# Kernel tuning notes

Hardware: AMD Instinct MI355X
Metric: run time of the kernel (lower is better)

## Reference

```python
import jax, jax.numpy as jnp
import numpy as np

H, I_, N, K, R, NL = 768, 1536, 16, 4, 48, 8
B, L, DIN = 4, 1024, 13
DA, RP = 128, 4
EPS = 1e-5

def _rmsnorm(x, w):
    v = jnp.mean(jnp.square(x), axis=-1, keepdims=True)
    return x * jax.lax.rsqrt(v + EPS) * w

def _causal_dwconv(hs, w, b):
    # hs: [B, I, L]; w: [I, K] depthwise kernel; causal (left) padding = K-1
    out = jax.lax.conv_general_dilated(
        hs, w[:, None, :], window_strides=(1,), padding=[(K - 1, 0)],
        dimension_numbers=('NCH', 'OIH', 'NCH'), feature_group_count=hs.shape[1])
    return out + b[None, :, None]

def _selective_scan(u, dt, Bm, Cm, A, D):
    # u, dt: [B, L, I]; Bm, Cm: [B, L, N]; A: [I, N]; D: [I]
    def step(h, inp):
        dt_t, B_t, C_t, u_t = inp          # [B,I], [B,N], [B,N], [B,I]
        dA = jnp.exp(dt_t[:, :, None] * A)  # [B,I,N]
        h = dA * h + (dt_t * u_t)[:, :, None] * B_t[:, None, :]
        y = jnp.einsum('bin,bn->bi', h, C_t)
        return h, y
    h0 = jnp.zeros((u.shape[0], A.shape[0], A.shape[1]), u.dtype)
    xs = (jnp.swapaxes(dt, 0, 1), jnp.swapaxes(Bm, 0, 1),
          jnp.swapaxes(Cm, 0, 1), jnp.swapaxes(u, 0, 1))
    _, ys = jax.lax.scan(step, h0, xs)
    return jnp.swapaxes(ys, 0, 1) + u * D

def _mamba_block(x, norm_w, in_w, conv_w, conv_b, xproj_w, dt_w, dt_b, A_log, D, out_w):
    res = x
    h = _rmsnorm(x, norm_w)
    proj = h @ in_w.T                      # [B,L,2I]
    hs, gate = jnp.split(proj, 2, axis=-1)
    hs = jnp.swapaxes(hs, 1, 2)            # [B,I,L]
    hs = jax.nn.silu(_causal_dwconv(hs, conv_w, conv_b))
    u = jnp.swapaxes(hs, 1, 2)             # [B,L,I]
    ssm = u @ xproj_w.T                    # [B,L,R+2N]
    ts, Bm, Cm = ssm[..., :R], ssm[..., R:R + N], ssm[..., R + N:]
    dt = jax.nn.softplus(ts @ dt_w.T + dt_b)
    y = _selective_scan(u, dt, Bm, Cm, -jnp.exp(A_log), D)
    y = y * jax.nn.silu(gate)
    return res + y @ out_w.T

def _forward(x, mlp_in_w1, mlp_in_b1, mlp_in_w2, mlp_in_b2, mlp_in_w3, mlp_in_b3,
             layers_norm_w, layers_in_proj_w, layers_conv_w, layers_conv_b,
             layers_x_proj_w, layers_dt_w, layers_dt_b, layers_A_log, layers_D,
             layers_out_proj_w, norm_f_w, attn_ws1, attn_ws2,
             mlp_out_w1, mlp_out_b1, mlp_out_w2, mlp_out_b2, mlp_out_w3, mlp_out_b3):
    h = jax.nn.relu(x @ mlp_in_w1.T + mlp_in_b1)
    h = jax.nn.relu(h @ mlp_in_w2.T + mlp_in_b2)
    h = h @ mlp_in_w3.T + mlp_in_b3        # [B,L,H]
    for l in range(NL):
        h = _mamba_block(h, layers_norm_w[l], layers_in_proj_w[l], layers_conv_w[l],
                         layers_conv_b[l], layers_x_proj_w[l], layers_dt_w[l],
                         layers_dt_b[l], layers_A_log[l], layers_D[l],
                         layers_out_proj_w[l])
    h = _rmsnorm(h, norm_f_w)              # final norm_f
    # attention pooling: softmax over the sequence dim (dim=1)
    attn = jax.nn.softmax(jnp.tanh(h @ attn_ws1.T) @ attn_ws2.T, axis=1)  # [B,L,r]
    m = jnp.einsum('blr,blh->brh', attn, h)  # bmm(attn^T, h) -> [B,r,H]
    flat = m.reshape(m.shape[0], -1)         # [B, r*H]
    o = jax.nn.relu(flat @ mlp_out_w1.T + mlp_out_b1)
    o = jax.nn.relu(o @ mlp_out_w2.T + mlp_out_b2)
    return o @ mlp_out_w3.T + mlp_out_b3     # [B,1]

def setup_inputs():
    key = jax.random.key(0)
    ks = iter(jax.random.split(key, 40))
    def nrm(shape, s=0.02):
        return jax.random.normal(next(ks), shape, dtype=jnp.float32) * s
    A_log = jnp.log(jnp.tile(jnp.arange(1, N + 1, dtype=jnp.float32)[None, None, :], (NL, I_, 1)))
    return {
        'x': jax.random.normal(next(ks), (B, L, DIN), dtype=jnp.float32),
        'mlp_in_w1': nrm((256, DIN)), 'mlp_in_b1': jnp.zeros((256,), jnp.float32),
        'mlp_in_w2': nrm((256, 256)), 'mlp_in_b2': jnp.zeros((256,), jnp.float32),
        'mlp_in_w3': nrm((H, 256)), 'mlp_in_b3': jnp.zeros((H,), jnp.float32),
        'layers_norm_w': jnp.ones((NL, H), jnp.float32),
        'layers_in_proj_w': nrm((NL, 2 * I_, H)),
        'layers_conv_w': nrm((NL, I_, K), 0.1),
        'layers_conv_b': jnp.zeros((NL, I_), jnp.float32),
        'layers_x_proj_w': nrm((NL, R + 2 * N, I_)),
        'layers_dt_w': nrm((NL, I_, R)),
        'layers_dt_b': jnp.full((NL, I_), -4.6, jnp.float32),
        'layers_A_log': A_log,
        'layers_D': jnp.ones((NL, I_), jnp.float32),
        'layers_out_proj_w': nrm((NL, H, I_)),
        'norm_f_w': jnp.ones((H,), jnp.float32),
        'attn_ws1': nrm((DA, H)), 'attn_ws2': nrm((RP, DA)),
        'mlp_out_w1': nrm((256, H * RP)), 'mlp_out_b1': jnp.zeros((256,), jnp.float32),
        'mlp_out_w2': nrm((256, 256)), 'mlp_out_b2': jnp.zeros((256,), jnp.float32),
        'mlp_out_w3': nrm((1, 256)), 'mlp_out_b3': jnp.zeros((1,), jnp.float32),
    }

def reference(x, mlp_in_w1, mlp_in_b1, mlp_in_w2, mlp_in_b2, mlp_in_w3, mlp_in_b3,
              layers_norm_w, layers_in_proj_w, layers_conv_w, layers_conv_b,
              layers_x_proj_w, layers_dt_w, layers_dt_b, layers_A_log, layers_D,
              layers_out_proj_w, norm_f_w, attn_ws1, attn_ws2,
              mlp_out_w1, mlp_out_b1, mlp_out_w2, mlp_out_b2, mlp_out_w3, mlp_out_b3):
    return _forward(x, mlp_in_w1, mlp_in_b1, mlp_in_w2, mlp_in_b2, mlp_in_w3, mlp_in_b3,
                    layers_norm_w, layers_in_proj_w, layers_conv_w, layers_conv_b,
                    layers_x_proj_w, layers_dt_w, layers_dt_b, layers_A_log, layers_D,
                    layers_out_proj_w, norm_f_w, attn_ws1, attn_ws2,
                    mlp_out_w1, mlp_out_b1, mlp_out_w2, mlp_out_b2, mlp_out_w3, mlp_out_b3)
```

## Files before the change

### kernel.cpp

```cpp
#include <hip/hip_runtime.h>
#include <cstddef>
#include <cstdint>

#define HD    768
#define ID    1536
#define ND    16
#define KD    4
#define RD    48
#define NLAY  8
#define BB    4
#define LL    1024
#define BL    4096
#define DIN   13
#define DA_   128
#define RP_   4

#define NC    32
#define CS    32

typedef _Float16 f16;
typedef f16 f16x8 __attribute__((ext_vector_type(8)));
typedef float f32x4 __attribute__((ext_vector_type(4)));

__device__ __forceinline__ float softplus_f(float x) {
    return (x > 20.f) ? x : log1pf(expf(x));
}

__device__ __forceinline__ float fast_exp2(float x) {
#if __has_builtin(__builtin_amdgcn_exp2f)
    return __builtin_amdgcn_exp2f(x);
#else
    return exp2f(x);
#endif
}

__global__ __launch_bounds__(256) void cast_f16_k(
    const float* __restrict__ in, f16* __restrict__ out, int n)
{
    int i = (blockIdx.x * 256 + threadIdx.x) * 4;
    if (i + 3 < n) {
        float4 v = *(const float4*)(in + i);
        out[i]     = (f16)v.x;
        out[i + 1] = (f16)v.y;
        out[i + 2] = (f16)v.z;
        out[i + 3] = (f16)v.w;
    } else {
        for (int j = i; j < n; ++j) out[j] = (f16)in[j];
    }
}

__global__ __launch_bounds__(256) void cast_dtw_k(
    const float* __restrict__ in, f16* __restrict__ out)
{
    int idx = blockIdx.x * 256 + threadIdx.x;
    if (idx >= NLAY * ID * 64) return;
    int k = idx & 63, r = idx >> 6;
    out[idx] = (k < RD) ? (f16)in[r * RD + k] : (f16)0.f;
}

__global__ __launch_bounds__(256) void zero_k(float* __restrict__ p, int n)
{
    int i = blockIdx.x * 256 + threadIdx.x;
    if (i < n) p[i] = 0.f;
}

__device__ __forceinline__ void epilogue_store(
    float v, int row, int col, int N,
    const float* __restrict__ res, int ldres,
    float* __restrict__ C, int ldc,
    f16* __restrict__ Cb, int ldcb, int ncb, int act,
    const float* __restrict__ bias)
{
    if (col >= N) return;
    if (bias) v += bias[col];
    if (act == 1) v = fmaxf(v, 0.f);
    else if (act == 2) v = tanhf(v);
    else if (act == 3) v = softplus_f(v);
    if (res) v += res[(size_t)row * ldres + col];
    if (C) C[(size_t)row * ldc + col] = v;
    if (Cb && col < ncb) Cb[(size_t)row * ldcb + col] = (f16)v;
}

__device__ __forceinline__ void async_copy16(const f16* g, f16* l) {
    __builtin_amdgcn_global_load_lds(
        (const __attribute__((address_space(1))) void*)g,
        (__attribute__((address_space(3))) void*)l, 16, 0, 0);
}

__global__ __launch_bounds__(256) void hgemm_k(
    const f16* __restrict__ A, int lda,
    const f16* __restrict__ W, int ldw,
    const float* __restrict__ bias,
    const float* __restrict__ res, int ldres,
    float* __restrict__ C, int ldc,
    f16* __restrict__ Cb, int ldcb, int ncb,
    int M, int N, int K, int act)
{
    __shared__ f16 As[128 * 64];
    __shared__ f16 Bs[128 * 64];
    int tid = threadIdx.x;
    int wave = tid >> 6, lane = tid & 63;
    int m0 = blockIdx.y * 128, n0 = blockIdx.x * 128;

    int wm = wave & 1, wn = wave >> 1;
    int lm = lane & 15;
    int kq = (lane >> 4) * 8;

    int srow = tid >> 2;
    int skc  = (tid & 3) * 8;

    f32x4 acc[4][4] = {};

    for (int k0 = 0; k0 < K; k0 += 64) {
#pragma unroll
        for (int it = 0; it < 4; ++it) {
            int rowo = (it & 1) * 64 + srow;
            int kk   = (it >> 1) * 32 + skc;
            int base = (it >> 1) * 4096 + (it & 1) * 2048 + wave * 512;
            async_copy16(A + (size_t)(m0 + rowo) * lda + k0 + kk, As + base);
            async_copy16(W + (size_t)(n0 + rowo) * ldw + k0 + kk, Bs + base);
        }
        __syncthreads();

        f16x8 af[4][2], bf[4][2];
#pragma unroll
        for (int ks = 0; ks < 2; ++ks) {
#pragma unroll
            for (int mt = 0; mt < 4; ++mt)
                af[mt][ks] = *(const f16x8*)(As + ks * 4096 +
                                 (wm * 64 + mt * 16 + lm) * 32 + kq);
#pragma unroll
            for (int nt = 0; nt < 4; ++nt)
                bf[nt][ks] = *(const f16x8*)(Bs + ks * 4096 +
                                 (wn * 64 + nt * 16 + lm) * 32 + kq);
        }
#pragma unroll
        for (int ks = 0; ks < 2; ++ks)
#pragma unroll
            for (int mt = 0; mt < 4; ++mt)
#pragma unroll
                for (int nt = 0; nt < 4; ++nt)
                    acc[mt][nt] = __builtin_amdgcn_mfma_f32_16x16x32_f16(
                        af[mt][ks], bf[nt][ks], acc[mt][nt], 0, 0, 0);
        __syncthreads();
    }

    int rq = (lane >> 4) * 4;
#pragma unroll
    for (int mt = 0; mt < 4; ++mt)
#pragma unroll
        for (int nt = 0; nt < 4; ++nt) {
            int col = n0 + wn * 64 + nt * 16 + lm;
#pragma unroll
            for (int r = 0; r < 4; ++r) {
                int row = m0 + wm * 64 + mt * 16 + rq + r;
                epilogue_store(acc[mt][nt][r], row, col, N, res, ldres,
                               C, ldc, Cb, ldcb, ncb, act, bias);
            }
        }
}

__global__ __launch_bounds__(256) void hgemm64_k(
    const f16* __restrict__ A, int lda,
    const f16* __restrict__ W, int ldw,
    const float* __restrict__ bias,
    const float* __restrict__ res, int ldres,
    float* __restrict__ C, int ldc,
    f16* __restrict__ Cb, int ldcb, int ncb,
    int M, int N, int K, int act)
{
    __shared__ f16 As[64 * 64];
    __shared__ f16 Bs[64 * 64];
    int tid = threadIdx.x;
    int wave = tid >> 6, lane = tid & 63;
    int m0 = blockIdx.y * 64, n0 = blockIdx.x * 64;

    int wm = wave & 1, wn = wave >> 1;
    int lm = lane & 15;
    int kq = (lane >> 4) * 8;

    int srow = tid >> 2;
    int skc  = (tid & 3) * 8;

    f32x4 acc[2][2] = {};

    for (int k0 = 0; k0 < K; k0 += 64) {
#pragma unroll
        for (int it = 0; it < 2; ++it) {
            int kk   = it * 32 + skc;
            int base = it * 2048 + wave * 512;
            async_copy16(A + (size_t)(m0 + srow) * lda + k0 + kk, As + base);
            async_copy16(W + (size_t)(n0 + srow) * ldw + k0 + kk, Bs + base);
        }
        __syncthreads();

        f16x8 af[2][2], bf[2][2];
#pragma unroll
        for (int ks = 0; ks < 2; ++ks) {
#pragma unroll
            for (int mt = 0; mt < 2; ++mt)
                af[mt][ks] = *(const f16x8*)(As + ks * 2048 +
                                 (wm * 32 + mt * 16 + lm) * 32 + kq);
#pragma unroll
            for (int nt = 0; nt < 2; ++nt)
                bf[nt][ks] = *(const f16x8*)(Bs + ks * 2048 +
                                 (wn * 32 + nt * 16 + lm) * 32 + kq);
        }
#pragma unroll
        for (int ks = 0; ks < 2; ++ks)
#pragma unroll
            for (int mt = 0; mt < 2; ++mt)
#pragma unroll
                for (int nt = 0; nt < 2; ++nt)
                    acc[mt][nt] = __builtin_amdgcn_mfma_f32_16x16x32_f16(
                        af[mt][ks], bf[nt][ks], acc[mt][nt], 0, 0, 0);
        __syncthreads();
    }

    int rq = (lane >> 4) * 4;
#pragma unroll
    for (int mt = 0; mt < 2; ++mt)
#pragma unroll
        for (int nt = 0; nt < 2; ++nt) {
            int col = n0 + wn * 32 + nt * 16 + lm;
#pragma unroll
            for (int r = 0; r < 4; ++r) {
                int row = m0 + wm * 32 + mt * 16 + rq + r;
                epilogue_store(acc[mt][nt][r], row, col, N, res, ldres,
                               C, ldc, Cb, ldcb, ncb, act, bias);
            }
        }
}

__global__ __launch_bounds__(256) void hgemm64s_k(
    const f16* __restrict__ A, int lda,
    const f16* __restrict__ W, int ldw,
    float* __restrict__ Cp, int ldc, size_t PS,
    int N, int kPer)
{
    __shared__ f16 As[64 * 64];
    __shared__ f16 Bs[64 * 64];
    int tid = threadIdx.x;
    int wave = tid >> 6, lane = tid & 63;
    int m0 = blockIdx.y * 64, n0 = blockIdx.x * 64;
    int z = blockIdx.z;
    int kbeg = z * kPer, kend = kbeg + kPer;

    int wm = wave & 1, wn = wave >> 1;
    int lm = lane & 15;
    int kq = (lane >> 4) * 8;
    int srow = tid >> 2;
    int skc  = (tid & 3) * 8;

    f32x4 acc[2][2] = {};

    for (int k0 = kbeg; k0 < kend; k0 += 64) {
#pragma unroll
        for (int it = 0; it < 2; ++it) {
            int kk   = it * 32 + skc;
            int base = it * 2048 + wave * 512;
            async_copy16(A + (size_t)(m0 + srow) * lda + k0 + kk, As + base);
            async_copy16(W + (size_t)(n0 + srow) * ldw + k0 + kk, Bs + base);
        }
        __syncthreads();

        f16x8 af[2][2], bf[2][2];
#pragma unroll
        for (int ks = 0; ks < 2; ++ks) {
#pragma unroll
            for (int mt = 0; mt < 2; ++mt)
                af[mt][ks] = *(const f16x8*)(As + ks * 2048 +
                                 (wm * 32 + mt * 16 + lm) * 32 + kq);
#pragma unroll
            for (int nt = 0; nt < 2; ++nt)
                bf[nt][ks] = *(const f16x8*)(Bs + ks * 2048 +
                                 (wn * 32 + nt * 16 + lm) * 32 + kq);
        }
#pragma unroll
        for (int ks = 0; ks < 2; ++ks)
#pragma unroll
            for (int mt = 0; mt < 2; ++mt)
#pragma unroll
                for (int nt = 0; nt < 2; ++nt)
                    acc[mt][nt] = __builtin_amdgcn_mfma_f32_16x16x32_f16(
                        af[mt][ks], bf[nt][ks], acc[mt][nt], 0, 0, 0);
        __syncthreads();
    }

    float* C = Cp + (size_t)z * PS;
    int rq = (lane >> 4) * 4;
#pragma unroll
    for (int mt = 0; mt < 2; ++mt)
#pragma unroll
        for (int nt = 0; nt < 2; ++nt) {
            int col = n0 + wn * 32 + nt * 16 + lm;
            if (col >= N) continue;
#pragma unroll
            for (int r = 0; r < 4; ++r) {
                int row = m0 + wm * 32 + mt * 16 + rq + r;
                C[(size_t)row * ldc + col] = acc[mt][nt][r];
            }
        }
}

__global__ __launch_bounds__(256) void xcomb_k(
    const float* __restrict__ part, float* __restrict__ ssm,
    f16* __restrict__ ssmb)
{
    int idx = blockIdx.x * 256 + threadIdx.x;
    if (idx >= BL * 96) return;
    int row = idx / 96, c = idx % 96;
    const size_t PS = (size_t)BL * 80;
    if (c < 80) {
        size_t o = (size_t)row * 80 + c;
        float s = part[o] + part[PS + o] + part[2 * PS + o] + part[3 * PS + o];
        ssm[o] = s;
        if (c < RD) ssmb[(size_t)row * 64 + c] = (f16)s;
    } else {
        ssmb[(size_t)row * 64 + (c - 80 + RD)] = (f16)0.f;
    }
}

#define BM 64
#define BN 64
#define BKK 16
__global__ __launch_bounds__(256) void gemm_k(
    const float* __restrict__ A, int lda,
    const float* __restrict__ W,
    const float* __restrict__ bias,
    float* __restrict__ C, int ldc,
    f16* __restrict__ Cb, int ldcb,
    int M, int N, int K, int act)
{
    __shared__ float As[BKK][BM + 4];
    __shared__ float Ws[BKK][BN + 4];
    int tid = threadIdx.x;
    int tx = tid & 15, ty = tid >> 4;
    int m0 = blockIdx.y * BM, n0 = blockIdx.x * BN;
    float acc[4][4] = {};
    int arow = tid >> 2;
    int acol = (tid & 3) * 4;

    for (int k0 = 0; k0 < K; k0 += BKK) {
        int gm = m0 + arow;
        int gn = n0 + arow;
#pragma unroll
        for (int j = 0; j < 4; ++j) {
            int gk = k0 + acol + j;
            float av = 0.f, wv = 0.f;
            if (gm < M && gk < K) av = A[(size_t)gm * lda + gk];
            if (gn < N && gk < K) wv = W[(size_t)gn * K + gk];
            As[acol + j][arow] = av;
            Ws[acol + j][arow] = wv;
        }
        __syncthreads();
#pragma unroll
        for (int k = 0; k < BKK; ++k) {
            float a[4], b[4];
#pragma unroll
            for (int i = 0; i < 4; ++i) a[i] = As[k][ty * 4 + i];
#pragma unroll
            for (int j = 0; j < 4; ++j) b[j] = Ws[k][tx * 4 + j];
#pragma unroll
            for (int i = 0; i < 4; ++i)
#pragma unroll
                for (int j = 0; j < 4; ++j)
                    acc[i][j] += a[i] * b[j];
        }
        __syncthreads();
    }

#pragma unroll
    for (int i = 0; i < 4; ++i) {
        int row = m0 + ty * 4 + i;
        if (row >= M) continue;
#pragma unroll
        for (int j = 0; j < 4; ++j) {
            int col = n0 + tx * 4 + j;
            if (col >= N) continue;
            float v = acc[i][j];
            if (bias) v += bias[col];
            if (act == 1) v = fmaxf(v, 0.f);
            if (C) C[(size_t)row * ldc + col] = v;
            if (Cb) Cb[(size_t)row * ldcb + col] = (f16)v;
        }
    }
}

__global__ __launch_bounds__(256) void rmsnorm_k(
    const float* __restrict__ x, const float* __restrict__ w,
    f16* __restrict__ out)
{
    int row = blockIdx.x;
    const float* xr = x + (size_t)row * HD;
    int tid = threadIdx.x;
    float v0 = xr[tid], v1 = xr[tid + 256], v2 = xr[tid + 512];
    __shared__ float red[256];
    red[tid] = v0 * v0 + v1 * v1 + v2 * v2;
    __syncthreads();
    for (int o = 128; o; o >>= 1) {
        if (tid < o) red[tid] += red[tid + o];
        __syncthreads();
    }
    float scale = rsqrtf(red[0] / (float)HD + 1e-5f);
    f16* outr = out + (size_t)row * HD;
    outr[tid]       = (f16)(v0 * scale * w[tid]);
    outr[tid + 256] = (f16)(v1 * scale * w[tid + 256]);
    outr[tid + 512] = (f16)(v2 * scale * w[tid + 512]);
}

__global__ __launch_bounds__(256) void conv_silu_k(
    const f16* __restrict__ projb, const float* __restrict__ cw,
    const float* __restrict__ cb, f16* __restrict__ ub)
{
    int idx = blockIdx.x * 256 + threadIdx.x;
    if (idx >= BL * (ID / 8)) return;
    int i8  = (idx % (ID / 8)) * 8;
    int row = idx / (ID / 8);
    int t = row & (LL - 1);

    float4 wv[8];
#pragma unroll
    for (int j = 0; j < 8; ++j)
        wv[j] = *(const float4*)(cw + (i8 + j) * KD);

    float s[8];
    float4 cb0 = *(const float4*)(cb + i8);
    float4 cb1 = *(const float4*)(cb + i8 + 4);
    s[0] = cb0.x; s[1] = cb0.y; s[2] = cb0.z; s[3] = cb0.w;
    s[4] = cb1.x; s[5] = cb1.y; s[6] = cb1.z; s[7] = cb1.w;

#pragma unroll
    for (int k = 0; k < KD; ++k) {
        int tt = t - (KD - 1) + k;
        if (tt < 0) continue;
        f16x8 p = *(const f16x8*)(projb + (size_t)(row - (KD - 1) + k) * (2 * ID) + i8);
#pragma unroll
        for (int j = 0; j < 8; ++j) {
            float wk = (k == 0) ? wv[j].x : (k == 1) ? wv[j].y
                     : (k == 2) ? wv[j].z : wv[j].w;
            s[j] += (float)p[j] * wk;
        }
    }
    f16x8 o;
#pragma unroll
    for (int j = 0; j < 8; ++j) {
        float v = s[j] / (1.f + expf(-s[j]));
        o[j] = (f16)v;
    }
    *(f16x8*)(ub + (size_t)row * ID + i8) = o;
}

__global__ __launch_bounds__(256) void scan1_k(
    const f16*   __restrict__ dtf,
    const float* __restrict__ ssm,
    const f16*   __restrict__ ub,
    const float* __restrict__ A_log,
    float* __restrict__ Pw, float* __restrict__ Hw)
{
    int b = blockIdx.z, c = blockIdx.y;
    int i = blockIdx.x * 256 + threadIdx.x;
    __shared__ float sB[CS * 16];
    for (int idx = threadIdx.x; idx < CS * 16; idx += 256) {
        int t = idx >> 4, n = idx & 15;
        sB[idx] = ssm[((size_t)(b * LL + c * CS + t)) * 80 + 48 + n];
    }
    __syncthreads();

    float Ain[16];
#pragma unroll
    for (int n = 0; n < 16; ++n)
        Ain[n] = -expf(A_log[i * ND + n]) * 1.44269504f;

    float h[16];
    float sdt = 0.f;
#pragma unroll
    for (int n = 0; n < 16; ++n) h[n] = 0.f;

    for (int t = 0; t < CS; ++t) {
        size_t row = (size_t)(b * LL + c * CS + t);
        float dtv = (float)dtf[row * ID + i];
        float x = dtv * (float)ub[row * ID + i];
        sdt += dtv;
        const float4* Bv = (const float4*)(sB + t * 16);
        float4 B0 = Bv[0], B1 = Bv[1], B2 = Bv[2], B3 = Bv[3];
        float Bf[16] = {B0.x, B0.y, B0.z, B0.w, B1.x, B1.y, B1.z, B1.w,
                        B2.x, B2.y, B2.z, B2.w, B3.x, B3.y, B3.z, B3.w};
#pragma unroll
        for (int n = 0; n < 16; ++n) {
            float dA = fast_exp2(dtv * Ain[n]);
            h[n] = dA * h[n] + x * Bf[n];
        }
    }
    size_t off = (((size_t)(b * NC + c) * ID + i) << 4);
    float4* pw = (float4*)(Pw + off);
    float4* hw = (float4*)(Hw + off);
#pragma unroll
    for (int q = 0; q < 4; ++q) {
        pw[q] = make_float4(fast_exp2(sdt * Ain[q*4]),
                            fast_exp2(sdt * Ain[q*4+1]),
                            fast_exp2(sdt * Ain[q*4+2]),
                            fast_exp2(sdt * Ain[q*4+3]));
        hw[q] = make_float4(h[q*4], h[q*4+1], h[q*4+2], h[q*4+3]);
    }
}

__global__ __launch_bounds__(256) void scan_comb_k(
    const float* __restrict__ Pw, float* __restrict__ Hw)
{
    int idx = blockIdx.x * 256 + threadIdx.x;
    int rem = idx & (ID * 16 - 1);
    int b = idx / (ID * 16);
    size_t base = (size_t)b * NC * ID * 16 + rem;
    float e = 0.f;
    for (int c = 0; c < NC; ++c) {
        size_t off = base + (size_t)c * ID * 16;
        float Hc = Hw[off];
        float Pc = Pw[off];
        Hw[off] = e;
        e = Hc + Pc * e;
    }
}

__global__ __launch_bounds__(256) void scan2_k(
    const f16*   __restrict__ dtf,
    const float* __restrict__ ssm,
    const f16*   __restrict__ ub,
    const f16*   __restrict__ projb,
    const float* __restrict__ A_log,
    const float* __restrict__ D,
    const float* __restrict__ Hw,
    f16* __restrict__ y)
{
    int b = blockIdx.z, c = blockIdx.y;
    int i = blockIdx.x * 256 + threadIdx.x;
    __shared__ float sB[CS * 16];
    __shared__ float sC[CS * 16];
    for (int idx = threadIdx.x; idx < CS * 16; idx += 256) {
        int t = idx >> 4, n = idx & 15;
        size_t row = (size_t)(b * LL + c * CS + t);
        sB[idx] = ssm[row * 80 + 48 + n];
        sC[idx] = ssm[row * 80 + 64 + n];
    }
    __syncthreads();

    float Ain[16];
#pragma unroll
    for (int n = 0; n < 16; ++n)
        Ain[n] = -expf(A_log[i * ND + n]) * 1.44269504f;
    float Dv = D[i];

    float h[16];
    size_t off = (((size_t)(b * NC + c) * ID + i) << 4);
    const float4* hw = (const float4*)(Hw + off);
#pragma unroll
    for (int q = 0; q < 4; ++q) {
        float4 v = hw[q];
        h[q*4] = v.x; h[q*4+1] = v.y; h[q*4+2] = v.z; h[q*4+3] = v.w;
    }

    for (int t = 0; t < CS; ++t) {
        size_t row = (size_t)(b * LL + c * CS + t);
        float dtv = (float)dtf[row * ID + i];
        float uv  = (float)ub[row * ID + i];
        float g   = (float)projb[row * (2 * ID) + ID + i];
        float x = dtv * uv;
        const float4* Bv = (const float4*)(sB + t * 16);
        const float4* Cv = (const float4*)(sC + t * 16);
        float4 B0 = Bv[0], B1 = Bv[1], B2 = Bv[2], B3 = Bv[3];
        float4 C0 = Cv[0], C1 = Cv[1], C2 = Cv[2], C3 = Cv[3];
        float Bf[16] = {B0.x, B0.y, B0.z, B0.w, B1.x, B1.y, B1.z, B1.w,
                        B2.x, B2.y, B2.z, B2.w, B3.x, B3.y, B3.z, B3.w};
        float Cf[16] = {C0.x, C0.y, C0.z, C0.w, C1.x, C1.y, C1.z, C1.w,
                        C2.x, C2.y, C2.z, C2.w, C3.x, C3.y, C3.z, C3.w};
        float yv = 0.f;
#pragma unroll
        for (int n = 0; n < 16; ++n) {
            float dA = fast_exp2(dtv * Ain[n]);
            h[n] = dA * h[n] + x * Bf[n];
            yv += h[n] * Cf[n];
        }
        yv = (yv + uv * Dv) * (g / (1.f + expf(-g)));
        y[row * ID + i] = (f16)yv;
    }
}

__global__ __launch_bounds__(256) void softmax_k(
    const float* __restrict__ s, float* __restrict__ attn)
{
    int b = blockIdx.x >> 2, r = blockIdx.x & 3;
    int tid = threadIdx.x;
    __shared__ float red[256];
    float mx = -1e30f;
    for (int j = 0; j < 4; ++j) {
        int t = tid + j * 256;
        mx = fmaxf(mx, s[((size_t)(b * LL + t)) * RP_ + r]);
    }
    red[tid] = mx;
    __syncthreads();
    for (int o = 128; o; o >>= 1) {
        if (tid < o) red[tid] = fmaxf(red[tid], red[tid + o]);
        __syncthreads();
    }
    mx = red[0];
    __syncthreads();
    float ev[4], sum = 0.f;
    for (int j = 0; j < 4; ++j) {
        int t = tid + j * 256;
        ev[j] = expf(s[((size_t)(b * LL + t)) * RP_ + r] - mx);
        sum += ev[j];
    }
    red[tid] = sum;
    __syncthreads();
    for (int o = 128; o; o >>= 1) {
        if (tid < o) red[tid] += red[tid + o];
        __syncthreads();
    }
    float inv = 1.f / red[0];
    for (int j = 0; j < 4; ++j) {
        int t = tid + j * 256;
        attn[((size_t)(b * LL + t)) * RP_ + r] = ev[j] * inv;
    }
}

__global__ __launch_bounds__(256) void pool_k(
    const float* __restrict__ attn, const f16* __restrict__ hn,
    float* __restrict__ m)
{
    int br = blockIdx.x;
    int b = br >> 2, r = br & 3;
    int t0 = blockIdx.y * 64;
    int tid = threadIdx.x;
    float acc0 = 0.f, acc1 = 0.f, acc2 = 0.f;
    for (int t = t0; t < t0 + 64; ++t) {
        float w = attn[((size_t)(b * LL + t)) * RP_ + r];
        const f16* hr = hn + ((size_t)(b * LL + t)) * HD;
        acc0 += w * (float)hr[tid];
        acc1 += w * (float)hr[tid + 256];
        acc2 += w * (float)hr[tid + 512];
    }
    float* outp = m + ((size_t)(b * RP_ + r)) * HD;
    atomicAdd(outp + tid, acc0);
    atomicAdd(outp + tid + 256, acc1);
    atomicAdd(outp + tid + 512, acc2);
}

__global__ __launch_bounds__(64) void gemv_k(
    const float* __restrict__ A, int lda,
    const float* __restrict__ W, const float* __restrict__ bias,
    float* __restrict__ C, int ldc, int K, int relu)
{
    int n = blockIdx.x, b = blockIdx.y;
    int lane = threadIdx.x;
    const float* a = A + (size_t)b * lda;
    const float* w = W + (size_t)n * K;
    float s = 0.f;
    for (int k = lane; k < K; k += 64) s += a[k] * w[k];
    for (int off = 32; off; off >>= 1) s += __shfl_down(s, off);
    if (lane == 0) {
        float v = s + (bias ? bias[n] : 0.f);
        if (relu) v = fmaxf(v, 0.f);
        C[(size_t)b * ldc + n] = v;
    }
}

extern "C" void kernel_launch(void* const* d_in, const int* in_sizes, int n_in,
                              void* d_out, int out_size, void* d_ws, size_t ws_size,
                              hipStream_t stream) {
    const float* x          = (const float*)d_in[0];
    const float* mlp_in_w1  = (const float*)d_in[1];
    const float* mlp_in_b1  = (const float*)d_in[2];
    const float* mlp_in_w2  = (const float*)d_in[3];
    const float* mlp_in_b2  = (const float*)d_in[4];
    const float* mlp_in_w3  = (const float*)d_in[5];
    const float* mlp_in_b3  = (const float*)d_in[6];
    const float* norm_w     = (const float*)d_in[7];
    const float* in_proj_w  = (const float*)d_in[8];
    const float* conv_w     = (const float*)d_in[9];
    const float* conv_b     = (const float*)d_in[10];
    const float* x_proj_w   = (const float*)d_in[11];
    const float* dt_w       = (const float*)d_in[12];
    const float* dt_b       = (const float*)d_in[13];
    const float* A_log      = (const float*)d_in[14];
    const float* Dp         = (const float*)d_in[15];
    const float* out_proj_w = (const float*)d_in[16];
    const float* norm_f_w   = (const float*)d_in[17];
    const float* attn_ws1   = (const float*)d_in[18];
    const float* attn_ws2   = (const float*)d_in[19];
    const float* mlp_out_w1 = (const float*)d_in[20];
    const float* mlp_out_b1 = (const float*)d_in[21];
    const float* mlp_out_w2 = (const float*)d_in[22];
    const float* mlp_out_b2 = (const float*)d_in[23];
    const float* mlp_out_w3 = (const float*)d_in[24];
    const float* mlp_out_b3 = (const float*)d_in[25];
    float* out = (float*)d_out;

    float* ws    = (float*)d_ws;
    float* h     = ws;
    float* ssm   = h    + (size_t)BL * HD;
    float* xpart = ssm  + (size_t)BL * 80;
    float* h1a   = xpart+ (size_t)4 * BL * 80;
    float* sbuf  = h1a  + (size_t)BL * DA_;
    float* attn  = sbuf + (size_t)BL * 4;
    float* mbuf  = attn + (size_t)BL * 4;
    float* o1    = mbuf + (size_t)BB * RP_ * HD;
    float* o2    = o1   + (size_t)BB * 256;
    float* Pw    = o2   + (size_t)BB * 256;
    float* Hw    = Pw   + (size_t)BB * NC * ID * 16;
    f16* fb    = (f16*)(Hw + (size_t)BB * NC * ID * 16);
    f16* h1b   = fb;
    f16* h2b   = h1b  + (size_t)BL * 256;
    f16* hnb   = h2b  + (size_t)BL * 256;
    f16* projb = hnb  + (size_t)BL * HD;
    f16* ub    = projb+ (size_t)BL * 2 * ID;
    f16* ssmb  = ub   + (size_t)BL * ID;
    f16* dtf   = ssmb + (size_t)BL * 64;
    f16* ybb   = dtf  + (size_t)BL * ID;
    f16* opwf  = ybb  + (size_t)BL * ID;
    f16* xpwf  = opwf + (size_t)NLAY * HD * ID;
    f16* dwwf  = xpwf + (size_t)NLAY * 80 * ID;
    f16* w2f   = dwwf + (size_t)NLAY * ID * 64;
    f16* w3f   = w2f  + 256 * 256;
    f16* a1f   = w3f  + HD * 256;
    f16* ipwf  = a1f  + DA_ * HD;

    size_t used_bytes = (size_t)((char*)(ipwf) - (char*)d_ws);
    size_t slot_bytes = (size_t)2 * ID * HD * sizeof(f16);
    int full = (ws_size >= used_bytes + (size_t)NLAY * slot_bytes) ? 1 : 0;

    dim3 blk(256);
    auto cgrid = [](int n) { return dim3((n / 4 + 255) / 256); };

    cast_f16_k<<<cgrid(256 * 256), blk, 0, stream>>>(mlp_in_w2, w2f, 256 * 256);
    cast_f16_k<<<cgrid(HD * 256), blk, 0, stream>>>(mlp_in_w3, w3f, HD * 256);
    cast_f16_k<<<cgrid(DA_ * HD), blk, 0, stream>>>(attn_ws1, a1f, DA_ * HD);
    cast_f16_k<<<cgrid(NLAY * HD * ID), blk, 0, stream>>>(out_proj_w, opwf, NLAY * HD * ID);
    cast_f16_k<<<cgrid(NLAY * 80 * ID), blk, 0, stream>>>(x_proj_w, xpwf, NLAY * 80 * ID);
    cast_dtw_k<<<(NLAY * ID * 64 + 255) / 256, blk, 0, stream>>>(dt_w, dwwf);
    if (full)
        cast_f16_k<<<cgrid(NLAY * 2 * ID * HD), blk, 0, stream>>>(
            in_proj_w, ipwf, NLAY * 2 * ID * HD);

    gemm_k<<<dim3(4, 64), blk, 0, stream>>>(
        x, DIN, mlp_in_w1, mlp_in_b1, nullptr, 0, h1b, 256, BL, 256, DIN, 1);
    hgemm64_k<<<dim3(4, 64), blk, 0, stream>>>(
        h1b, 256, w2f, 256, mlp_in_b2, nullptr, 0, nullptr, 0, h2b, 256, 256,
        BL, 256, 256, 1);
    hgemm64_k<<<dim3(12, 64), blk, 0, stream>>>(
        h2b, 256, w3f, 256, mlp_in_b3, nullptr, 0, h, HD, nullptr, 0, 0,
        BL, HD, 256, 0);

    for (int l = 0; l < NLAY; ++l) {
        const float* nw  = norm_w + (size_t)l * HD;
        const float* cw  = conv_w + (size_t)l * ID * KD;
        const float* cb  = conv_b + (size_t)l * ID;
        const float* db  = dt_b   + (size_t)l * ID;
        const float* al  = A_log  + (size_t)l * ID * ND;
        const float* dv  = Dp     + (size_t)l * ID;

        const f16* ipw;
        if (full) {
            ipw = ipwf + (size_t)l * 2 * ID * HD;
        } else {
            cast_f16_k<<<cgrid(2 * ID * HD), blk, 0, stream>>>(
                in_proj_w + (size_t)l * 2 * ID * HD, ipwf, 2 * ID * HD);
            ipw = ipwf;
        }
        rmsnorm_k<<<BL, blk, 0, stream>>>(h, nw, hnb);
        hgemm_k<<<dim3(24, 32), blk, 0, stream>>>(
            hnb, HD, ipw, HD, nullptr, nullptr, 0, nullptr, 0,
            projb, 2 * ID, 2 * ID, BL, 2 * ID, HD, 0);
        conv_silu_k<<<(BL * (ID / 8) + 255) / 256, blk, 0, stream>>>(
            projb, cw, cb, ub);

        hgemm64s_k<<<dim3(2, 64, 4), blk, 0, stream>>>(
            ub, ID, xpwf + (size_t)l * 80 * ID, ID,
            xpart, 80, (size_t)BL * 80, 80, ID / 4);
        xcomb_k<<<(BL * 96 + 255) / 256, blk, 0, stream>>>(xpart, ssm, ssmb);

        hgemm64_k<<<dim3(24, 64), blk, 0, stream>>>(
            ssmb, 64, dwwf + (size_t)l * ID * 64, 64, db, nullptr, 0,
            nullptr, 0, dtf, ID, ID, BL, ID, 64, 3);

        scan1_k<<<dim3(ID / 256, NC, BB), blk, 0, stream>>>(
            dtf, ssm, ub, al, Pw, Hw);
        scan_comb_k<<<(BB * ID * 16) / 256, blk, 0, stream>>>(Pw, Hw);
        scan2_k<<<dim3(ID / 256, NC, BB), blk, 0, stream>>>(
            dtf, ssm, ub, projb, al, dv, Hw, ybb);

        hgemm64_k<<<dim3(12, 64), blk, 0, stream>>>(
            ybb, ID, opwf + (size_t)l * HD * ID, ID, nullptr, h, HD,
            h, HD, nullptr, 0, 0, BL, HD, ID, 0);
    }

    rmsnorm_k<<<BL, blk, 0, stream>>>(h, norm_f_w, hnb);
    hgemm64_k<<<dim3(2, 64), blk, 0, stream>>>(
        hnb, HD, a1f, HD, nullptr, nullptr, 0, h1a, DA_, nullptr, 0, 0,
        BL, DA_, HD, 2);
    gemm_k<<<dim3(1, 64), blk, 0, stream>>>(
        h1a, DA_, attn_ws2, nullptr, sbuf, RP_, nullptr, 0, BL, RP_, DA_, 0);
    softmax_k<<<BB * RP_, blk, 0, stream>>>(sbuf, attn);
    zero_k<<<(BB * RP_ * HD + 255) / 256, blk, 0, stream>>>(mbuf, BB * RP_ * HD);
    pool_k<<<dim3(BB * RP_, LL / 64), blk, 0, stream>>>(attn, hnb, mbuf);

    gemv_k<<<dim3(256, BB), dim3(64), 0, stream>>>(
        mbuf, RP_ * HD, mlp_out_w1, mlp_out_b1, o1, 256, RP_ * HD, 1);
    gemv_k<<<dim3(256, BB), dim3(64), 0, stream>>>(
        o1, 256, mlp_out_w2, mlp_out_b2, o2, 256, 256, 1);
    gemv_k<<<dim3(1, BB), dim3(64), 0, stream>>>(
        o2, 256, mlp_out_w3, mlp_out_b3, out, 1, 256, 0);
}
```

Before: 2.247 ms.

## Double-buffer LDS tiles in HGEMM kernels to overlap loads with MFMA

```diff
diff --git a/kernel.cpp b/kernel.cpp
--- a/kernel.cpp
+++ b/kernel.cpp
@@ -96,8 +96,8 @@
     f16* __restrict__ Cb, int ldcb, int ncb,
     int M, int N, int K, int act)
 {
-    __shared__ f16 As[128 * 64];
-    __shared__ f16 Bs[128 * 64];
+    __shared__ f16 As[2][128 * 32];
+    __shared__ f16 Bs[2][128 * 32];
     int tid = threadIdx.x;
     int wave = tid >> 6, lane = tid & 63;
     int m0 = blockIdx.y * 128, n0 = blockIdx.x * 128;
@@ -106,43 +106,51 @@
     int lm = lane & 15;
     int kq = (lane >> 4) * 8;
 
-    int srow = tid >> 2;
-    int skc  = (tid & 3) * 8;
+    int srow = lane >> 2;
+    int skc  = (lane & 3) * 8;
 
     f32x4 acc[4][4] = {};
 
-    for (int k0 = 0; k0 < K; k0 += 64) {
-#pragma unroll
-        for (int it = 0; it < 4; ++it) {
-            int rowo = (it & 1) * 64 + srow;
-            int kk   = (it >> 1) * 32 + skc;
-            int base = (it >> 1) * 4096 + (it & 1) * 2048 + wave * 512;
-            async_copy16(A + (size_t)(m0 + rowo) * lda + k0 + kk, As + base);
-            async_copy16(W + (size_t)(n0 + rowo) * ldw + k0 + kk, Bs + base);
-        }
+    int nIter = K >> 5;
+
+#pragma unroll
+    for (int it = 0; it < 2; ++it) {
+        int c16 = wave + it * 4;
+        int row = c16 * 16 + srow;
+        async_copy16(A + (size_t)(m0 + row) * lda + skc, As[0] + c16 * 512);
+        async_copy16(W + (size_t)(n0 + row) * ldw + skc, Bs[0] + c16 * 512);
+    }
+
+    for (int i = 0; i < nIter; ++i) {
         __syncthreads();
-
-        f16x8 af[4][2], bf[4][2];
-#pragma unroll
-        for (int ks = 0; ks < 2; ++ks) {
-#pragma unroll
-            for (int mt = 0; mt < 4; ++mt)
-                af[mt][ks] = *(const f16x8*)(As + ks * 4096 +
-                                 (wm * 64 + mt * 16 + lm) * 32 + kq);
+        if (i + 1 < nIter) {
+            int k0 = (i + 1) << 5;
+            int nb = (i + 1) & 1;
+#pragma unroll
+            for (int it = 0; it < 2; ++it) {
+                int c16 = wave + it * 4;
+                int row = c16 * 16 + srow;
+                async_copy16(A + (size_t)(m0 + row) * lda + k0 + skc,
+                             As[nb] + c16 * 512);
+                async_copy16(W + (size_t)(n0 + row) * ldw + k0 + skc,
+                             Bs[nb] + c16 * 512);
+            }
+        }
+        const f16* ab = As[i & 1];
+        const f16* bb = Bs[i & 1];
+        f16x8 af[4], bf[4];
+#pragma unroll
+        for (int mt = 0; mt < 4; ++mt)
+            af[mt] = *(const f16x8*)(ab + (wm * 64 + mt * 16 + lm) * 32 + kq);
+#pragma unroll
+        for (int nt = 0; nt < 4; ++nt)
+            bf[nt] = *(const f16x8*)(bb + (wn * 64 + nt * 16 + lm) * 32 + kq);
+#pragma unroll
+        for (int mt = 0; mt < 4; ++mt)
 #pragma unroll
             for (int nt = 0; nt < 4; ++nt)
-                bf[nt][ks] = *(const f16x8*)(Bs + ks * 4096 +
-                                 (wn * 64 + nt * 16 + lm) * 32 + kq);
-        }
-#pragma unroll
-        for (int ks = 0; ks < 2; ++ks)
-#pragma unroll
-            for (int mt = 0; mt < 4; ++mt)
-#pragma unroll
-                for (int nt = 0; nt < 4; ++nt)
-                    acc[mt][nt] = __builtin_amdgcn_mfma_f32_16x16x32_f16(
-                        af[mt][ks], bf[nt][ks], acc[mt][nt], 0, 0, 0);
-        __syncthreads();
+                acc[mt][nt] = __builtin_amdgcn_mfma_f32_16x16x32_f16(
+                    af[mt], bf[nt], acc[mt][nt], 0, 0, 0);
     }
 
     int rq = (lane >> 4) * 4;
@@ -169,8 +177,8 @@
     f16* __restrict__ Cb, int ldcb, int ncb,
     int M, int N, int K, int act)
 {
-    __shared__ f16 As[64 * 64];
-    __shared__ f16 Bs[64 * 64];
+    __shared__ f16 As[2][64 * 64];
+    __shared__ f16 Bs[2][64 * 64];
     int tid = threadIdx.x;
     int wave = tid >> 6, lane = tid & 63;
     int m0 = blockIdx.y * 64, n0 = blockIdx.x * 64;
@@ -183,27 +191,43 @@
     int skc  = (tid & 3) * 8;
 
     f32x4 acc[2][2] = {};
-
-    for (int k0 = 0; k0 < K; k0 += 64) {
-#pragma unroll
-        for (int it = 0; it < 2; ++it) {
-            int kk   = it * 32 + skc;
-            int base = it * 2048 + wave * 512;
-            async_copy16(A + (size_t)(m0 + srow) * lda + k0 + kk, As + base);
-            async_copy16(W + (size_t)(n0 + srow) * ldw + k0 + kk, Bs + base);
-        }
+    int nIter = K >> 6;
+
+#pragma unroll
+    for (int it = 0; it < 2; ++it) {
+        int kk   = it * 32 + skc;
+        int base = it * 2048 + wave * 512;
+        async_copy16(A + (size_t)(m0 + srow) * lda + kk, As[0] + base);
+        async_copy16(W + (size_t)(n0 + srow) * ldw + kk, Bs[0] + base);
+    }
+
+    for (int i = 0; i < nIter; ++i) {
         __syncthreads();
-
+        if (i + 1 < nIter) {
+            int k0 = (i + 1) << 6;
+            int nb = (i + 1) & 1;
+#pragma unroll
+            for (int it = 0; it < 2; ++it) {
+                int kk   = it * 32 + skc;
+                int base = it * 2048 + wave * 512;
+                async_copy16(A + (size_t)(m0 + srow) * lda + k0 + kk,
+                             As[nb] + base);
+                async_copy16(W + (size_t)(n0 + srow) * ldw + k0 + kk,
+                             Bs[nb] + base);
+            }
+        }
+        const f16* ab = As[i & 1];
+        const f16* bb = Bs[i & 1];
         f16x8 af[2][2], bf[2][2];
 #pragma unroll
         for (int ks = 0; ks < 2; ++ks) {
 #pragma unroll
             for (int mt = 0; mt < 2; ++mt)
-                af[mt][ks] = *(const f16x8*)(As + ks * 2048 +
+                af[mt][ks] = *(const f16x8*)(ab + ks * 2048 +
                                  (wm * 32 + mt * 16 + lm) * 32 + kq);
 #pragma unroll
             for (int nt = 0; nt < 2; ++nt)
-                bf[nt][ks] = *(const f16x8*)(Bs + ks * 2048 +
+                bf[nt][ks] = *(const f16x8*)(bb + ks * 2048 +
                                  (wn * 32 + nt * 16 + lm) * 32 + kq);
         }
 #pragma unroll
@@ -214,7 +238,6 @@
                 for (int nt = 0; nt < 2; ++nt)
                     acc[mt][nt] = __builtin_amdgcn_mfma_f32_16x16x32_f16(
                         af[mt][ks], bf[nt][ks], acc[mt][nt], 0, 0, 0);
-        __syncthreads();
     }
 
     int rq = (lane >> 4) * 4;
@@ -238,13 +261,13 @@
     float* __restrict__ Cp, int ldc, size_t PS,
     int N, int kPer)
 {
-    __shared__ f16 As[64 * 64];
-    __shared__ f16 Bs[64 * 64];
+    __shared__ f16 As[2][64 * 64];
+    __shared__ f16 Bs[2][64 * 64];
     int tid = threadIdx.x;
     int wave = tid >> 6, lane = tid & 63;
     int m0 = blockIdx.y * 64, n0 = blockIdx.x * 64;
     int z = blockIdx.z;
-    int kbeg = z * kPer, kend = kbeg + kPer;
+    int kbeg = z * kPer;
 
     int wm = wave & 1, wn = wave >> 1;
     int lm = lane & 15;
@@ -253,27 +276,43 @@
     int skc  = (tid & 3) * 8;
 
     f32x4 acc[2][2] = {};
-
-    for (int k0 = kbeg; k0 < kend; k0 += 64) {
-#pragma unroll
-        for (int it = 0; it < 2; ++it) {
-            int kk   = it * 32 + skc;
-            int base = it * 2048 + wave * 512;
-            async_copy16(A + (size_t)(m0 + srow) * lda + k0 + kk, As + base);
-            async_copy16(W + (size_t)(n0 + srow) * ldw + k0 + kk, Bs + base);
-        }
+    int nIter = kPer >> 6;
+
+#pragma unroll
+    for (int it = 0; it < 2; ++it) {
+        int kk   = it * 32 + skc;
+        int base = it * 2048 + wave * 512;
+        async_copy16(A + (size_t)(m0 + srow) * lda + kbeg + kk, As[0] + base);
+        async_copy16(W + (size_t)(n0 + srow) * ldw + kbeg + kk, Bs[0] + base);
+    }
+
+    for (int i = 0; i < nIter; ++i) {
         __syncthreads();
-
+        if (i + 1 < nIter) {
+            int k0 = kbeg + ((i + 1) << 6);
+            int nb = (i + 1) & 1;
+#pragma unroll
+            for (int it = 0; it < 2; ++it) {
+                int kk   = it * 32 + skc;
+                int base = it * 2048 + wave * 512;
+                async_copy16(A + (size_t)(m0 + srow) * lda + k0 + kk,
+                             As[nb] + base);
+                async_copy16(W + (size_t)(n0 + srow) * ldw + k0 + kk,
+                             Bs[nb] + base);
+            }
+        }
+        const f16* ab = As[i & 1];
+        const f16* bb = Bs[i & 1];
         f16x8 af[2][2], bf[2][2];
 #pragma unroll
         for (int ks = 0; ks < 2; ++ks) {
 #pragma unroll
             for (int mt = 0; mt < 2; ++mt)
-                af[mt][ks] = *(const f16x8*)(As + ks * 2048 +
+                af[mt][ks] = *(const f16x8*)(ab + ks * 2048 +
                                  (wm * 32 + mt * 16 + lm) * 32 + kq);
 #pragma unroll
             for (int nt = 0; nt < 2; ++nt)
-                bf[nt][ks] = *(const f16x8*)(Bs + ks * 2048 +
+                bf[nt][ks] = *(const f16x8*)(bb + ks * 2048 +
                                  (wn * 32 + nt * 16 + lm) * 32 + kq);
         }
 #pragma unroll
@@ -284,7 +323,6 @@
                 for (int nt = 0; nt < 2; ++nt)
                     acc[mt][nt] = __builtin_amdgcn_mfma_f32_16x16x32_f16(
                         af[mt][ks], bf[nt][ks], acc[mt][nt], 0, 0, 0);
-        __syncthreads();
     }
 
     float* C = Cp + (size_t)z * PS;
```

Result: no change. 2.249 ms (+0.1%).
